# Kernel optimization log

Hardware: AMD Instinct MI355X
Metric: run time of the kernel (lower is better)

## Reference

```python
import jax, jax.numpy as jnp
import numpy as np

EPS = 1e-8          # smoothing_radius
REF_AREA = 1.0      # reference_area
NB, NS, NF, NPTS = 2, 2, 512, 1024   # n_bc_types, n_ref_lengths, faces per BC, query points
NLS, NLV, H, F = 12, 6, 64, 29       # latent scalars, latent vectors, hidden, pair-feature dim


def _legendre4(c):
    # First 4 Legendre polynomials of cos(angle) -- n_spherical_harmonics=4
    return jnp.stack([jnp.ones_like(c), c, 0.5 * (3.0 * c * c - 1.0),
                      0.5 * (5.0 * c ** 3 - 3.0 * c)], axis=-1)


def _mlp(x, W1, b1, W2, b2, W3, b3, Wo, bo):
    h = jax.nn.silu(x @ W1 + b1)
    h = jax.nn.silu(h @ W2 + b2)
    h = jax.nn.silu(h @ W3 + b3)
    return h @ Wo + bo


def _pair_feats(tgt, pos, nrm, scal, vecs, L):
    # tgt [T,3], pos/nrm [S,3], scal [S,NLS], vecs [S,NLV,3], L scalar
    rvec = tgt[:, None, :] - pos[None, :, :]                    # [T,S,3]
    r = jnp.sqrt(jnp.sum(rvec * rvec, axis=-1) + EPS * EPS)     # [T,S]
    rhat = rvec / r[..., None]
    cos = jnp.einsum('tsd,sd->ts', rhat, nrm)
    leg = _legendre4(cos)                                       # [T,S,4]
    logr = jnp.log(r / L)[..., None]                            # [T,S,1]
    T, S = rhat.shape[0], pos.shape[0]
    sc = jnp.broadcast_to(scal[None], (T, S, NLS))
    vr = jnp.einsum('tsd,svd->tsv', rhat, vecs)                 # [T,S,NLV]
    vn = jnp.broadcast_to(jnp.einsum('svd,sd->sv', vecs, nrm)[None], (T, S, NLV))
    feats = jnp.concatenate([logr, leg, sc, vr, vn], axis=-1)   # [T,S,29]
    return feats, rhat


def setup_inputs() -> dict:
    key = jax.random.key(0)
    ks = jax.random.split(key, 24)
    wi = (2.0 / F) ** 0.5
    wh = (2.0 / H) ** 0.5
    rn = lambda k, shp, s: jax.random.normal(ks[k], shp, jnp.float32) * s
    return {
        'prediction_points': rn(0, (NPTS, 3), 1.0),
        'centroids': rn(1, (NB, NF, 3), 1.0),
        'normals': rn(2, (NB, NF, 3), 1.0),
        'areas': jax.random.uniform(ks[3], (NB, NF), jnp.float32) + 0.1,
        'ref_lengths': jax.random.uniform(ks[4], (NS,), jnp.float32) + 0.5,
        'cW1': rn(5, (2, NB, NS, F, H), wi), 'cb1': jnp.zeros((2, NB, NS, H), jnp.float32),
        'cW2': rn(6, (2, NB, NS, H, H), wh), 'cb2': jnp.zeros((2, NB, NS, H), jnp.float32),
        'cW3': rn(7, (2, NB, NS, H, H), wh), 'cb3': jnp.zeros((2, NB, NS, H), jnp.float32),
        'cWo': rn(8, (2, NB, NS, H, NLS + 2 * NLV), 0.1), 'cbo': jnp.zeros((2, NB, NS, NLS + 2 * NLV), jnp.float32),
        'fW1': rn(9, (NB, NS, F, H), wi), 'fb1': jnp.zeros((NB, NS, H), jnp.float32),
        'fW2': rn(10, (NB, NS, H, H), wh), 'fb2': jnp.zeros((NB, NS, H), jnp.float32),
        'fW3': rn(11, (NB, NS, H, H), wh), 'fb3': jnp.zeros((NB, NS, H), jnp.float32),
        'fWo': rn(12, (NB, NS, H, 3), 0.1), 'fbo': jnp.zeros((NB, NS, 3), jnp.float32),
        'calib': rn(13, (3,), 1.0),
    }


def reference(prediction_points, centroids, normals, areas, ref_lengths,
              cW1, cb1, cW2, cb2, cW3, cb3, cWo, cbo,
              fW1, fb1, fW2, fb2, fW3, fb3, fWo, fbo, calib):
    nrm = normals / jnp.linalg.norm(normals, axis=-1, keepdims=True)
    w = areas / REF_AREA                                        # [NB,NF]
    all_pos = centroids.reshape(-1, 3)                          # all boundary faces as targets
    scal = jnp.zeros((NB, NF, NLS), jnp.float32)
    vecs = jnp.zeros((NB, NF, NLV, 3), jnp.float32)

    # communication hyperlayers: boundary -> boundary
    for layer in range(2):
        ns = jnp.zeros((NB * NF, NLS), jnp.float32)
        nv = jnp.zeros((NB * NF, NLV, 3), jnp.float32)
        for b in range(NB):
            for s in range(NS):
                feats, rhat = _pair_feats(all_pos, centroids[b], nrm[b], scal[b], vecs[b], ref_lengths[s])
                out = _mlp(feats, cW1[layer, b, s], cb1[layer, b, s], cW2[layer, b, s], cb2[layer, b, s],
                           cW3[layer, b, s], cb3[layer, b, s], cWo[layer, b, s], cbo[layer, b, s])
                cs = out[..., :NLS]
                cr = out[..., NLS:NLS + NLV]
                cn = out[..., NLS + NLV:]
                ns = ns + jnp.einsum('tsk,s->tk', cs, w[b])
                nv = nv + jnp.einsum('tsv,s,tsd->tvd', cr, w[b], rhat) \
                        + jnp.einsum('tsv,s,sd->tvd', cn, w[b], nrm[b])
        scal = ns.reshape(NB, NF, NLS)
        vecs = nv.reshape(NB, NF, NLV, 3)

    # final hyperlayer: boundary -> query points
    p = jnp.zeros((prediction_points.shape[0],), jnp.float32)
    v = jnp.zeros((prediction_points.shape[0], 3), jnp.float32)
    for b in range(NB):
        for s in range(NS):
            feats, rhat = _pair_feats(prediction_points, centroids[b], nrm[b], scal[b], vecs[b], ref_lengths[s])
            out = _mlp(feats, fW1[b, s], fb1[b, s], fW2[b, s], fb2[b, s],
                       fW3[b, s], fb3[b, s], fWo[b, s], fbo[b, s])            # [T,S,3]
            p = p + jnp.einsum('ts,s->t', out[..., 0], w[b])
            v = v + jnp.einsum('ts,s,tsd->td', out[..., 1], w[b], rhat) \
                  + jnp.einsum('ts,s,sd->td', out[..., 2], w[b], nrm[b])

    # per-field calibration: affine for scalar, scale-only (equivariant) for vector
    p = calib[0] * p + calib[1]
    v = calib[2] * v
    return jnp.concatenate([p[:, None], v], axis=-1)            # [NPTS,4]
```

## Files before the change

### kernel.cpp

```cpp
#include <hip/hip_runtime.h>
#include <hip/hip_bf16.h>

constexpr int kNB = 2, kNS = 2, kNF = 512, kNPTS = 1024;
constexpr int kNLS = 12, kNLV = 6;
constexpr int kNTGT = kNB * kNF;

typedef float f32x4 __attribute__((ext_vector_type(4)));
typedef short bf16x8 __attribute__((ext_vector_type(8)));

constexpr int kWperMLP = 12288;
constexpr int kBperMLP = 224;

__device__ __forceinline__ unsigned short f2bf(float x) {
  union { float f; unsigned u; } v;
  v.f = x;
  unsigned r = v.u + 0x7fffu + ((v.u >> 16) & 1u);
  return (unsigned short)(r >> 16);
}
__device__ __forceinline__ float bf2f(short b) {
  union { unsigned u; float f; } v;
  v.u = ((unsigned)(unsigned short)b) << 16;
  return v.f;
}
__device__ __forceinline__ unsigned pk2(float a, float b) {
  union { __hip_bfloat162 h2; unsigned u; } cv;
  cv.h2.x = __float2bfloat16(a);
  cv.h2.y = __float2bfloat16(b);
  return cv.u;
}
__device__ __forceinline__ float silu_f(float t) {
  return t * __builtin_amdgcn_rcpf(1.0f + __expf(-t));
}
__device__ __forceinline__ float wred64(float v) {
#pragma unroll
  for (int off = 32; off > 0; off >>= 1) v += __shfl_xor(v, off, 64);
  return v;
}

__global__ void prep_nrm(const float* __restrict__ normals,
                         float* __restrict__ nrm) {
  const int i = blockIdx.x * blockDim.x + threadIdx.x;
  if (i < kNTGT) {
    const float x = normals[i * 3 + 0], y = normals[i * 3 + 1],
                z = normals[i * 3 + 2];
    const float inv = rsqrtf(x * x + y * y + z * z);
    nrm[i * 3 + 0] = x * inv;
    nrm[i * 3 + 1] = y * inv;
    nrm[i * 3 + 2] = z * inv;
  }
}

template <int KR, int NR, int KP, int NP>
__global__ void prep_w(const float* __restrict__ src, short* __restrict__ dst,
                       int woff, int nmats, int mlp0) {
  constexpr int NCT = NP / 16, NF = KP / 32, NFRAG = NCT * NF;
  const int i = blockIdx.x * blockDim.x + threadIdx.x;
  if (i >= nmats * NFRAG * 64) return;
  const int lane = i & 63;
  const int frag = (i >> 6) % NFRAG;
  const int mat = i / (64 * NFRAG);
  const int ct = frag / NF, f = frag % NF;
  const int k0 = 32 * f + 8 * (lane >> 4);
  const int n = 16 * ct + (lane & 15);
  bf16x8 o;
#pragma unroll
  for (int p = 0; p < 8; ++p) {
    const int k = k0 + p;
    const float v = (k < KR && n < NR) ? src[(mat * KR + k) * NR + n] : 0.f;
    o[p] = (short)f2bf(v);
  }
  *(bf16x8*)(dst + (long)(mlp0 + mat) * kWperMLP + woff + frag * 512 +
             lane * 8) = o;
}

__global__ void prep_b(const float* __restrict__ src, float* __restrict__ dst,
                       int nmats, int NRr, int NPp, int off, int mlp0) {
  const int i = blockIdx.x * blockDim.x + threadIdx.x;
  if (i >= nmats * NPp) return;
  const int mat = i / NPp, j = i % NPp;
  dst[(mlp0 + mat) * kBperMLP + off + j] = (j < NRr) ? src[mat * NRr + j] : 0.f;
}

template <bool FIRST, bool FINAL>
__global__ __launch_bounds__(512, 2) void mlp_main(
    const float* __restrict__ tgt, const float* __restrict__ cent,
    const float* __restrict__ nrm, const float* __restrict__ areas,
    const float* __restrict__ refl, const short* __restrict__ WL,
    const float* __restrict__ BL, int mlp0, const float* __restrict__ scal_in,
    const float* __restrict__ vecs_in, float* __restrict__ scal_out,
    float* __restrict__ vecs_out, const float* __restrict__ calib,
    float* __restrict__ out4) {
  __shared__ short Xb[512 * 32];
  __shared__ short Hb[512 * 64];
  __shared__ float red[8 * 32];
  char* Xc = (char*)Xb;
  char* Hc = (char*)Hb;
  const int tid = threadIdx.x;
  const int lane = tid & 63;
  const int c15 = lane & 15, q = lane >> 4;
  const int wave = tid >> 6;
  const int t = blockIdx.x;
  const float tx = tgt[t * 3 + 0], ty = tgt[t * 3 + 1], tz = tgt[t * 3 + 2];
  const int m = tid;
  const int mf = wave * 64 + c15;

  constexpr int NACC = FINAL ? 4 : 30;
  float acc[NACC];
#pragma unroll
  for (int k = 0; k < NACC; ++k) acc[k] = 0.f;

#pragma unroll 1
  for (int bs = 0; bs < 4; ++bs) {
    const int b = bs >> 1, s = bs & 1;
    const short* wb = WL + (long)(mlp0 + bs) * kWperMLP;
    const float* bb = BL + (mlp0 + bs) * kBperMLP;

    const int sg = b * kNF + m;
    const float px = cent[sg * 3 + 0], py = cent[sg * 3 + 1],
                pz = cent[sg * 3 + 2];
    const float nx = nrm[sg * 3 + 0], ny = nrm[sg * 3 + 1],
                nz = nrm[sg * 3 + 2];
    const float wgt = areas[sg];
    const float rvx = tx - px, rvy = ty - py, rvz = tz - pz;
    const float r = sqrtf(rvx * rvx + rvy * rvy + rvz * rvz + 1e-16f);
    const float rinv = 1.f / r;
    const float rhx = rvx * rinv, rhy = rvy * rinv, rhz = rvz * rinv;
    const float cth = rhx * nx + rhy * ny + rhz * nz;
    {
      float f[32];
      f[0] = __logf(r / refl[s]);
      f[1] = 1.f;
      f[2] = cth;
      f[3] = 0.5f * (3.f * cth * cth - 1.f);
      f[4] = 0.5f * cth * (5.f * cth * cth - 3.f);
      if constexpr (!FIRST) {
#pragma unroll
        for (int k = 0; k < kNLS; ++k) f[5 + k] = scal_in[sg * kNLS + k];
#pragma unroll
        for (int v = 0; v < kNLV; ++v) {
          const float vx = vecs_in[sg * 18 + v * 3 + 0];
          const float vy = vecs_in[sg * 18 + v * 3 + 1];
          const float vz = vecs_in[sg * 18 + v * 3 + 2];
          f[17 + v] = rhx * vx + rhy * vy + rhz * vz;
          f[23 + v] = nx * vx + ny * vy + nz * vz;
        }
      } else {
#pragma unroll
        for (int k = 5; k < 29; ++k) f[k] = 0.f;
      }
      f[29] = f[30] = f[31] = 0.f;
#pragma unroll
      for (int g = 0; g < 8; ++g) {
        uint2 u;
        u.x = pk2(f[4 * g + 0], f[4 * g + 1]);
        u.y = pk2(f[4 * g + 2], f[4 * g + 3]);
        *(uint2*)(Xc + ((m * 64 + 8 * g) ^ ((m & 3) << 4))) = u;
      }
    }

    {
      bf16x8 w1[4];
      f32x4 bv[4];
#pragma unroll
      for (int ct = 0; ct < 4; ++ct) {
        w1[ct] = *(const bf16x8*)(wb + ct * 512 + lane * 8);
        bv[ct] = *(const f32x4*)(bb + 16 * ct + 4 * q);
      }
      f32x4 a[4][4];
#pragma unroll
      for (int rt = 0; rt < 4; ++rt) {
        const int mr = mf + rt * 16;
        const bf16x8 xf =
            *(const bf16x8*)(Xc + ((mr * 64 + 16 * q) ^ ((mr & 3) << 4)));
#pragma unroll
        for (int ct = 0; ct < 4; ++ct)
          a[rt][ct] = __builtin_amdgcn_mfma_f32_16x16x32_bf16(w1[ct], xf,
                                                              bv[ct], 0, 0, 0);
      }
#pragma unroll
      for (int rt = 0; rt < 4; ++rt) {
        const int mr = mf + rt * 16;
#pragma unroll
        for (int ct = 0; ct < 4; ++ct) {
          f32x4 v = a[rt][ct];
          uint2 u;
          u.x = pk2(silu_f(v.x), silu_f(v.y));
          u.y = pk2(silu_f(v.z), silu_f(v.w));
          *(uint2*)(Hc + ((mr * 128 + 32 * ct + 8 * q) ^ ((mr & 7) << 4))) = u;
        }
      }
    }

#pragma unroll 1
    for (int L = 0; L < 2; ++L) {
      const int woff = (L == 0) ? 2048 : 6144;
      const int boff = (L == 0) ? 64 : 128;
      bf16x8 w[4][2];
      f32x4 bv[4];
#pragma unroll
      for (int ct = 0; ct < 4; ++ct) {
        w[ct][0] = *(const bf16x8*)(wb + woff + (ct * 2 + 0) * 512 + lane * 8);
        w[ct][1] = *(const bf16x8*)(wb + woff + (ct * 2 + 1) * 512 + lane * 8);
        bv[ct] = *(const f32x4*)(bb + boff + 16 * ct + 4 * q);
      }
      f32x4 a[4][4];
#pragma unroll
      for (int rt = 0; rt < 4; ++rt) {
        const int mr = mf + rt * 16;
        const bf16x8 h0 =
            *(const bf16x8*)(Hc + ((mr * 128 + 16 * q) ^ ((mr & 7) << 4)));
        const bf16x8 h1 =
            *(const bf16x8*)(Hc + ((mr * 128 + 64 + 16 * q) ^ ((mr & 7) << 4)));
#pragma unroll
        for (int ct = 0; ct < 4; ++ct) {
          f32x4 aa = __builtin_amdgcn_mfma_f32_16x16x32_bf16(w[ct][0], h0,
                                                             bv[ct], 0, 0, 0);
          aa = __builtin_amdgcn_mfma_f32_16x16x32_bf16(w[ct][1], h1, aa, 0, 0,
                                                       0);
          a[rt][ct] = aa;
        }
      }
#pragma unroll
      for (int rt = 0; rt < 4; ++rt) {
        const int mr = mf + rt * 16;
#pragma unroll
        for (int ct = 0; ct < 4; ++ct) {
          f32x4 v = a[rt][ct];
          uint2 u;
          u.x = pk2(silu_f(v.x), silu_f(v.y));
          u.y = pk2(silu_f(v.z), silu_f(v.w));
          *(uint2*)(Hc + ((mr * 128 + 32 * ct + 8 * q) ^ ((mr & 7) << 4))) = u;
        }
      }
    }

    {
      constexpr int NCTO = FINAL ? 1 : 2;
      bf16x8 wo[NCTO][2];
      f32x4 bv[NCTO];
#pragma unroll
      for (int ct = 0; ct < NCTO; ++ct) {
        wo[ct][0] =
            *(const bf16x8*)(wb + 10240 + (ct * 2 + 0) * 512 + lane * 8);
        wo[ct][1] =
            *(const bf16x8*)(wb + 10240 + (ct * 2 + 1) * 512 + lane * 8);
        bv[ct] = *(const f32x4*)(bb + 192 + 16 * ct + 4 * q);
      }
#pragma unroll
      for (int rt = 0; rt < 4; ++rt) {
        const int mr = mf + rt * 16;
        const bf16x8 h0 =
            *(const bf16x8*)(Hc + ((mr * 128 + 16 * q) ^ ((mr & 7) << 4)));
        const bf16x8 h1 =
            *(const bf16x8*)(Hc + ((mr * 128 + 64 + 16 * q) ^ ((mr & 7) << 4)));
#pragma unroll
        for (int ct = 0; ct < NCTO; ++ct) {
          f32x4 aa = __builtin_amdgcn_mfma_f32_16x16x32_bf16(wo[ct][0], h0,
                                                             bv[ct], 0, 0, 0);
          aa = __builtin_amdgcn_mfma_f32_16x16x32_bf16(wo[ct][1], h1, aa, 0, 0,
                                                       0);
          uint2 u;
          u.x = pk2(aa.x, aa.y);
          u.y = pk2(aa.z, aa.w);
          *(uint2*)(Xc + ((mr * 64 + 32 * ct + 8 * q) ^ ((mr & 3) << 4))) = u;
        }
      }
    }

    if constexpr (!FINAL) {
      float o[24];
#pragma unroll
      for (int j = 0; j < 3; ++j) {
        const bf16x8 v =
            *(const bf16x8*)(Xc + ((m * 64 + 16 * j) ^ ((m & 3) << 4)));
#pragma unroll
        for (int i = 0; i < 8; ++i) o[8 * j + i] = bf2f(v[i]);
      }
#pragma unroll
      for (int k = 0; k < kNLS; ++k) acc[k] += o[k] * wgt;
#pragma unroll
      for (int v = 0; v < kNLV; ++v) {
        const float cr = o[12 + v] * wgt, cn = o[18 + v] * wgt;
        acc[12 + v * 3 + 0] += cr * rhx + cn * nx;
        acc[12 + v * 3 + 1] += cr * rhy + cn * ny;
        acc[12 + v * 3 + 2] += cr * rhz + cn * nz;
      }
    } else {
      const bf16x8 v = *(const bf16x8*)(Xc + ((m * 64) ^ ((m & 3) << 4)));
      const float o0 = bf2f(v[0]), o1 = bf2f(v[1]), o2 = bf2f(v[2]);
      acc[0] += o0 * wgt;
      acc[1] += wgt * (o1 * rhx + o2 * nx);
      acc[2] += wgt * (o1 * rhy + o2 * ny);
      acc[3] += wgt * (o1 * rhz + o2 * nz);
    }
  }

#pragma unroll
  for (int k = 0; k < NACC; ++k) acc[k] = wred64(acc[k]);
  if (lane == 0) {
#pragma unroll
    for (int k = 0; k < NACC; ++k) red[wave * 32 + k] = acc[k];
  }
  __syncthreads();
  if (tid < NACC) {
    float sum = 0.f;
#pragma unroll
    for (int w = 0; w < 8; ++w) sum += red[w * 32 + tid];
    if constexpr (!FINAL) {
      if (tid < kNLS)
        scal_out[t * kNLS + tid] = sum;
      else
        vecs_out[t * 18 + (tid - kNLS)] = sum;
    } else {
      const float o =
          (tid == 0) ? (calib[0] * sum + calib[1]) : (calib[2] * sum);
      out4[t * 4 + tid] = o;
    }
  }
}

extern "C" void kernel_launch(void* const* d_in, const int* in_sizes, int n_in,
                              void* d_out, int out_size, void* d_ws,
                              size_t ws_size, hipStream_t stream) {
  const float* pred = (const float*)d_in[0];
  const float* cent = (const float*)d_in[1];
  const float* normals = (const float*)d_in[2];
  const float* areas = (const float*)d_in[3];
  const float* refl = (const float*)d_in[4];
  const float* cW1 = (const float*)d_in[5];
  const float* cb1 = (const float*)d_in[6];
  const float* cW2 = (const float*)d_in[7];
  const float* cb2 = (const float*)d_in[8];
  const float* cW3 = (const float*)d_in[9];
  const float* cb3 = (const float*)d_in[10];
  const float* cWo = (const float*)d_in[11];
  const float* cbo = (const float*)d_in[12];
  const float* fW1 = (const float*)d_in[13];
  const float* fb1 = (const float*)d_in[14];
  const float* fW2 = (const float*)d_in[15];
  const float* fb2 = (const float*)d_in[16];
  const float* fW3 = (const float*)d_in[17];
  const float* fb3 = (const float*)d_in[18];
  const float* fWo = (const float*)d_in[19];
  const float* fbo = (const float*)d_in[20];
  const float* calib = (const float*)d_in[21];

  float* ws = (float*)d_ws;
  float* nrmp = ws;
  float* scalA = nrmp + 3072;
  float* vecsA = scalA + 12288;
  float* scalB = vecsA + 18432;
  float* vecsB = scalB + 12288;
  float* BLs = vecsB + 18432;
  short* WLs = (short*)(BLs + 2688);
  float* outp = (float*)d_out;

  prep_nrm<<<4, 256, 0, stream>>>(normals, nrmp);

  prep_w<29, 64, 32, 64><<<8, 256, 0, stream>>>(cW1, WLs, 0, 8, 0);
  prep_w<64, 64, 64, 64><<<16, 256, 0, stream>>>(cW2, WLs, 2048, 8, 0);
  prep_w<64, 64, 64, 64><<<16, 256, 0, stream>>>(cW3, WLs, 6144, 8, 0);
  prep_w<64, 24, 64, 32><<<8, 256, 0, stream>>>(cWo, WLs, 10240, 8, 0);
  prep_w<29, 64, 32, 64><<<4, 256, 0, stream>>>(fW1, WLs, 0, 4, 8);
  prep_w<64, 64, 64, 64><<<8, 256, 0, stream>>>(fW2, WLs, 2048, 4, 8);
  prep_w<64, 64, 64, 64><<<8, 256, 0, stream>>>(fW3, WLs, 6144, 4, 8);
  prep_w<64, 3, 64, 32><<<4, 256, 0, stream>>>(fWo, WLs, 10240, 4, 8);

  prep_b<<<2, 256, 0, stream>>>(cb1, BLs, 8, 64, 64, 0, 0);
  prep_b<<<2, 256, 0, stream>>>(cb2, BLs, 8, 64, 64, 64, 0);
  prep_b<<<2, 256, 0, stream>>>(cb3, BLs, 8, 64, 64, 128, 0);
  prep_b<<<1, 256, 0, stream>>>(cbo, BLs, 8, 24, 32, 192, 0);
  prep_b<<<1, 256, 0, stream>>>(fb1, BLs, 4, 64, 64, 0, 8);
  prep_b<<<1, 256, 0, stream>>>(fb2, BLs, 4, 64, 64, 64, 8);
  prep_b<<<1, 256, 0, stream>>>(fb3, BLs, 4, 64, 64, 128, 8);
  prep_b<<<1, 256, 0, stream>>>(fbo, BLs, 4, 3, 32, 192, 8);

  mlp_main<true, false><<<kNTGT, 512, 0, stream>>>(
      cent, cent, nrmp, areas, refl, WLs, BLs, 0, nullptr, nullptr, scalA,
      vecsA, nullptr, nullptr);
  mlp_main<false, false><<<kNTGT, 512, 0, stream>>>(
      cent, cent, nrmp, areas, refl, WLs, BLs, 4, scalA, vecsA, scalB, vecsB,
      nullptr, nullptr);
  mlp_main<false, true><<<kNPTS, 512, 0, stream>>>(
      pred, cent, nrmp, areas, refl, WLs, BLs, 8, scalB, vecsB, nullptr,
      nullptr, calib, outp);
}
```

Baseline: 496.2 us.

## Split each target's work across four (b,s) blocks with separate reduction kernels

```diff
diff --git a/kernel.cpp b/kernel.cpp
--- a/kernel.cpp
+++ b/kernel.cpp
@@ -10,6 +10,7 @@
 
 constexpr int kWperMLP = 12288;
 constexpr int kBperMLP = 224;
+constexpr int kPSTR = 32;
 
 __device__ __forceinline__ unsigned short f2bf(float x) {
   union { float f; unsigned u; } v;
@@ -81,25 +82,52 @@
   dst[(mlp0 + mat) * kBperMLP + off + j] = (j < NRr) ? src[mat * NRr + j] : 0.f;
 }
 
+__global__ void reduce_moments(const float* __restrict__ part,
+                               float* __restrict__ scal_out,
+                               float* __restrict__ vecs_out) {
+  const int i = blockIdx.x * blockDim.x + threadIdx.x;
+  if (i >= kNTGT * 30) return;
+  const int t = i / 30, k = i % 30;
+  float s = 0.f;
+#pragma unroll
+  for (int bs = 0; bs < 4; ++bs) s += part[(bs * kNTGT + t) * kPSTR + k];
+  if (k < kNLS)
+    scal_out[t * kNLS + k] = s;
+  else
+    vecs_out[t * 18 + (k - kNLS)] = s;
+}
+
+__global__ void reduce_final(const float* __restrict__ part,
+                             const float* __restrict__ calib,
+                             float* __restrict__ out4) {
+  const int i = blockIdx.x * blockDim.x + threadIdx.x;
+  if (i >= kNPTS * 4) return;
+  const int t = i >> 2, k = i & 3;
+  float s = 0.f;
+#pragma unroll
+  for (int bs = 0; bs < 4; ++bs) s += part[(bs * kNPTS + t) * 4 + k];
+  out4[i] = (k == 0) ? (calib[0] * s + calib[1]) : (calib[2] * s);
+}
+
 template <bool FIRST, bool FINAL>
-__global__ __launch_bounds__(512, 2) void mlp_main(
+__global__ __launch_bounds__(256, 2) void mlp_main(
     const float* __restrict__ tgt, const float* __restrict__ cent,
     const float* __restrict__ nrm, const float* __restrict__ areas,
     const float* __restrict__ refl, const short* __restrict__ WL,
     const float* __restrict__ BL, int mlp0, const float* __restrict__ scal_in,
-    const float* __restrict__ vecs_in, float* __restrict__ scal_out,
-    float* __restrict__ vecs_out, const float* __restrict__ calib,
-    float* __restrict__ out4) {
-  __shared__ short Xb[512 * 32];
-  __shared__ short Hb[512 * 64];
-  __shared__ float red[8 * 32];
+    const float* __restrict__ vecs_in, float* __restrict__ part) {
+  __shared__ short Xb[256 * 32];
+  __shared__ short Hb[256 * 64];
+  __shared__ float red[4 * 32];
   char* Xc = (char*)Xb;
   char* Hc = (char*)Hb;
   const int tid = threadIdx.x;
   const int lane = tid & 63;
   const int c15 = lane & 15, q = lane >> 4;
   const int wave = tid >> 6;
-  const int t = blockIdx.x;
+  const int t = blockIdx.x & (FINAL ? (kNPTS - 1) : (kNTGT - 1));
+  const int bs = blockIdx.x >> 10;
+  const int b = bs >> 1, s = bs & 1;
   const float tx = tgt[t * 3 + 0], ty = tgt[t * 3 + 1], tz = tgt[t * 3 + 2];
   const int m = tid;
   const int mf = wave * 64 + c15;
@@ -109,13 +137,12 @@
 #pragma unroll
   for (int k = 0; k < NACC; ++k) acc[k] = 0.f;
 
+  const short* wb = WL + (long)(mlp0 + bs) * kWperMLP;
+  const float* bb = BL + (mlp0 + bs) * kBperMLP;
+
 #pragma unroll 1
-  for (int bs = 0; bs < 4; ++bs) {
-    const int b = bs >> 1, s = bs & 1;
-    const short* wb = WL + (long)(mlp0 + bs) * kWperMLP;
-    const float* bb = BL + (mlp0 + bs) * kBperMLP;
-
-    const int sg = b * kNF + m;
+  for (int half = 0; half < 2; ++half) {
+    const int sg = b * kNF + half * 256 + m;
     const float px = cent[sg * 3 + 0], py = cent[sg * 3 + 1],
                 pz = cent[sg * 3 + 2];
     const float nx = nrm[sg * 3 + 0], ny = nrm[sg * 3 + 1],
@@ -305,17 +332,11 @@
   if (tid < NACC) {
     float sum = 0.f;
 #pragma unroll
-    for (int w = 0; w < 8; ++w) sum += red[w * 32 + tid];
-    if constexpr (!FINAL) {
-      if (tid < kNLS)
-        scal_out[t * kNLS + tid] = sum;
-      else
-        vecs_out[t * 18 + (tid - kNLS)] = sum;
-    } else {
-      const float o =
-          (tid == 0) ? (calib[0] * sum + calib[1]) : (calib[2] * sum);
-      out4[t * 4 + tid] = o;
-    }
+    for (int w = 0; w < 4; ++w) sum += red[w * 32 + tid];
+    if constexpr (!FINAL)
+      part[(bs * kNTGT + t) * kPSTR + tid] = sum;
+    else
+      part[(bs * kNPTS + t) * 4 + tid] = sum;
   }
 }
 
@@ -352,7 +373,9 @@
   float* scalB = vecsA + 18432;
   float* vecsB = scalB + 12288;
   float* BLs = vecsB + 18432;
-  short* WLs = (short*)(BLs + 2688);
+  float* partM = BLs + 2688;
+  float* partF = partM + 4 * kNTGT * kPSTR;
+  short* WLs = (short*)(partF + 4 * kNPTS * 4);
   float* outp = (float*)d_out;
 
   prep_nrm<<<4, 256, 0, stream>>>(normals, nrmp);
@@ -375,13 +398,16 @@
   prep_b<<<1, 256, 0, stream>>>(fb3, BLs, 4, 64, 64, 128, 8);
   prep_b<<<1, 256, 0, stream>>>(fbo, BLs, 4, 3, 32, 192, 8);
 
-  mlp_main<true, false><<<kNTGT, 512, 0, stream>>>(
-      cent, cent, nrmp, areas, refl, WLs, BLs, 0, nullptr, nullptr, scalA,
-      vecsA, nullptr, nullptr);
-  mlp_main<false, false><<<kNTGT, 512, 0, stream>>>(
-      cent, cent, nrmp, areas, refl, WLs, BLs, 4, scalA, vecsA, scalB, vecsB,
-      nullptr, nullptr);
-  mlp_main<false, true><<<kNPTS, 512, 0, stream>>>(
-      pred, cent, nrmp, areas, refl, WLs, BLs, 8, scalB, vecsB, nullptr,
-      nullptr, calib, outp);
-}
+  mlp_main<true, false><<<4 * kNTGT, 256, 0, stream>>>(
+      cent, cent, nrmp, areas, refl, WLs, BLs, 0, nullptr, nullptr, partM);
+  reduce_moments<<<(kNTGT * 30 + 255) / 256, 256, 0, stream>>>(partM, scalA,
+                                                               vecsA);
+  mlp_main<false, false><<<4 * kNTGT, 256, 0, stream>>>(
+      cent, cent, nrmp, areas, refl, WLs, BLs, 4, scalA, vecsA, partM);
+  reduce_moments<<<(kNTGT * 30 + 255) / 256, 256, 0, stream>>>(partM, scalB,
+                                                               vecsB);
+  mlp_main<false, true><<<4 * kNPTS, 256, 0, stream>>>(
+      pred, cent, nrmp, areas, refl, WLs, BLs, 8, scalB, vecsB, partF);
+  reduce_final<<<(kNPTS * 4 + 255) / 256, 256, 0, stream>>>(partF, calib,
+                                                            outp);
+}
```

Result: faster. 484.9 us (-2.3%).
